# Kernel tuning notes

Hardware: AMD Instinct MI355X
Metric: run time of the kernel (lower is better)

The kernel has to match this reference:

```python
import jax, jax.numpy as jnp
import numpy as np

N_QUBITS = 18
LAYERS = 6
DATA_REUPLOADING = True


def _apply_1q(state, gate, q, n):
    # state: [2^n] complex, gate: [2,2] complex, acts on qubit q (big-endian)
    s = state.reshape(2 ** q, 2, 2 ** (n - q - 1))
    s = jnp.einsum('ab,ibj->iaj', gate, s)
    return s.reshape(-1)


def _apply_cz_adj(state, q, n):
    # CZ on adjacent qubits (q, q+1): flip sign of |..11..> amplitudes
    s = state.reshape(2 ** q, 2, 2, 2 ** (n - q - 2))
    s = s.at[:, 1, 1, :].multiply(-1.0)
    return s.reshape(-1)


def _rx(t):
    c = jnp.cos(t / 2).astype(jnp.complex64)
    s = (-1j * jnp.sin(t / 2)).astype(jnp.complex64)
    return jnp.stack([jnp.stack([c, s]), jnp.stack([s, c])])


def _ry(t):
    c = jnp.cos(t / 2).astype(jnp.complex64)
    s = jnp.sin(t / 2).astype(jnp.complex64)
    return jnp.stack([jnp.stack([c, -s]), jnp.stack([s, c])])


def _rz(t):
    em = jnp.exp(-1j * t.astype(jnp.complex64) / 2)
    ep = jnp.exp(1j * t.astype(jnp.complex64) / 2)
    z = jnp.zeros((), jnp.complex64)
    return jnp.stack([jnp.stack([em, z]), jnp.stack([z, ep])])


def _circuit(x, input_scaling, variational):
    # Hardware-efficient ansatz: RX(data) encoding, RY+RZ variational, CZ chain
    n = N_QUBITS
    state = jnp.zeros(2 ** n, jnp.complex64).at[0].set(1.0)
    for l in range(LAYERS):
        if l == 0 or DATA_REUPLOADING:
            for q in range(n):
                state = _apply_1q(state, _rx(input_scaling[l, q] * x[q]), q, n)
        for q in range(n):
            state = _apply_1q(state, _ry(variational[l, q]), q, n)
        for q in range(n):
            state = _apply_1q(state, _rz(variational[l, n + q]), q, n)
        for q in range(n - 1):
            state = _apply_cz_adj(state, q, n)
    return state


def setup_inputs() -> dict:
    key = jax.random.key(0)
    k1, k2, k3 = jax.random.split(key, 3)
    x1 = jax.random.normal(k1, (N_QUBITS,), jnp.float32)
    x2 = jax.random.normal(k2, (N_QUBITS,), jnp.float32)
    input_scaling = jnp.ones((LAYERS, N_QUBITS), jnp.float32)
    variational = (jax.random.uniform(k3, (LAYERS, 2 * N_QUBITS), jnp.float32)
                   * 2 * np.pi - np.pi)
    return {"x1": x1, "x2": x2, "input_scaling": input_scaling,
            "variational": variational}


def reference(x1, x2, input_scaling, variational):
    psi1 = _circuit(x1, input_scaling, variational)
    psi2 = _circuit(x2, input_scaling, variational)
    # projector |0><0| expectation of U(x2)^dagger U(x1)|0> == |<psi2|psi1>|^2
    ov = jnp.vdot(psi2, psi1)
    return (ov.real ** 2 + ov.imag ** 2).astype(jnp.float32)
```

## Files before the change

kernel.cpp:

```cpp
#include <hip/hip_runtime.h>
#include <math.h>


#define NQ      18
#define NSTATE  (1 << NQ)
#define TPB     512
#define MAGIC   0x5EED5EEDu

__device__ __forceinline__ int SW(int i) { return i ^ ((i >> 5) & 31); }

__device__ __forceinline__ float2 cmulf(float2 a, float2 b) {
    return make_float2(a.x * b.x - a.y * b.y, a.x * b.y + a.y * b.x);
}

__device__ __forceinline__ float lxor(float x, int j) {
    if (j == 0) {
        int v = __float_as_int(x);
        return __int_as_float(__builtin_amdgcn_update_dpp(v, v, 0xB1, 0xF, 0xF, false));
    }
    if (j == 1) {
        int v = __float_as_int(x);
        return __int_as_float(__builtin_amdgcn_update_dpp(v, v, 0x4E, 0xF, 0xF, false));
    }
    return __shfl_xor(x, 1 << j, 64);
}

__device__ __forceinline__ void cpair(
    float& a0r, float& a0i, float& a1r, float& a1i,
    float u00r, float u00i, float u01r, float u01i,
    float u10r, float u10i, float u11r, float u11i)
{
    float n0r = u00r * a0r - u00i * a0i + u01r * a1r - u01i * a1i;
    float n0i = u00r * a0i + u00i * a0r + u01r * a1i + u01i * a1r;
    float n1r = u10r * a0r - u10i * a0i + u11r * a1r - u11i * a1i;
    float n1i = u10r * a0i + u10i * a0r + u11r * a1i + u11i * a1r;
    a0r = n0r; a0i = n0i; a1r = n1r; a1i = n1i;
}

template<int RB>
__device__ __forceinline__ void reg_gate4(float (&ar)[4], float (&ai)[4],
                                          const float2* up)
{
    float u00r = up[0].x, u00i = up[0].y, u01r = up[1].x, u01i = up[1].y;
    float u10r = up[2].x, u10i = up[2].y, u11r = up[3].x, u11i = up[3].y;
#pragma unroll
    for (int r = 0; r < 4; ++r) {
        if (r & RB) continue;
        int r1 = r | RB;
        cpair(ar[r], ai[r], ar[r1], ai[r1],
              u00r, u00i, u01r, u01i, u10r, u10i, u11r, u11i);
    }
}

__device__ __forceinline__ void lane_gate4(float (&ar)[4], float (&ai)[4],
                                           const float2* up, int lane, int j)
{
    float u00r = up[0].x, u00i = up[0].y, u01r = up[1].x, u01i = up[1].y;
    float u10r = up[2].x, u10i = up[2].y, u11r = up[3].x, u11i = up[3].y;
    int side = (lane >> j) & 1;
    float car = side ? u11r : u00r, cai = side ? u11i : u00i;
    float cbr = side ? u10r : u01r, cbi = side ? u10i : u01i;
#pragma unroll
    for (int r = 0; r < 4; ++r) {
        float pr = lxor(ar[r], j);
        float pi = lxor(ai[r], j);
        float mr = ar[r], mi = ai[r];
        ar[r] = car * mr - cai * mi + cbr * pr - cbi * pi;
        ai[r] = car * mi + cai * mr + cbr * pi + cbi * pr;
    }
}

__global__ __launch_bounds__(TPB) void sim_kernel(
    float2* __restrict__ states,
    const float* __restrict__ x1, const float* __restrict__ x2,
    const float* __restrict__ iscale, const float* __restrict__ var,
    double* __restrict__ acc, unsigned* __restrict__ cnt,
    unsigned* __restrict__ flags, float* __restrict__ out)
{
    __shared__ float sre[2048], sim_[2048];
    __shared__ float2 sUa[5 * 11 * 4];
    __shared__ float2 sUb[5 * 11 * 4];
    __shared__ float2 sDa[6 * 4];
    __shared__ float2 sDb[11 * 4];
    __shared__ double wr[8], wi[8];

    int blk = blockIdx.x, t = threadIdx.x, lane = t & 63, wave = t >> 6;
    int c = blk >> 7, gc = blk & 127;
    int wv0 = wave & 1, wv1 = (wave >> 1) & 1, wv2 = (wave >> 2) & 1;
    const float* xv = c ? x2 : x1;

    if (blk == 0 && t == 0) {
        acc[0] = 0.0; acc[1] = 0.0; *cnt = 0u;
        __hip_atomic_store(&flags[128 * 16], MAGIC, __ATOMIC_RELEASE,
                           __HIP_MEMORY_SCOPE_AGENT);
    }

    if (t < 110) {
        int which = t >= 55;
        int tt = which ? t - 55 : t;
        int l = tt / 11, w = tt % 11;
        int q = which ? (17 - w) : (10 - w);
        float tx = iscale[l * NQ + q] * xv[q];
        float ty = var[l * 2 * NQ + q];
        float tz = var[l * 2 * NQ + NQ + q];
        float sx, cx, sy, cy, sz, cz;
        sincosf(tx * 0.5f, &sx, &cx);
        sincosf(ty * 0.5f, &sy, &cy);
        sincosf(tz * 0.5f, &sz, &cz);
        float m00r = cy * cx,  m00i =  sy * sx;
        float m01r = -sy * cx, m01i = -cy * sx;
        float m10r = sy * cx,  m10i = -cy * sx;
        float m11r = cy * cx,  m11i = -sy * sx;
        float2* up = which ? &sUb[(l * 11 + w) * 4] : &sUa[(l * 11 + w) * 4];
        up[0] = make_float2(m00r * cz + m00i * sz, m00i * cz - m00r * sz);
        up[1] = make_float2(m01r * cz + m01i * sz, m01i * cz - m01r * sz);
        up[2] = make_float2(m10r * cz - m10i * sz, m10i * cz + m10r * sz);
        up[3] = make_float2(m11r * cz - m11i * sz, m11i * cz + m11r * sz);
    } else if (t < 127) {
        int isb = t >= 116;
        int j = isb ? (t - 116) : (t - 110);
        int q = isb ? (17 - j) : (5 - j);
        float d = iscale[5 * NQ + q] * (x1[q] - x2[q]);
        float sn, cs;
        sincosf(d * 0.5f, &sn, &cs);
        float2* up = isb ? &sDb[j * 4] : &sDa[j * 4];
        up[0] = make_float2(cs, 0.f);  up[1] = make_float2(0.f, sn);
        up[2] = make_float2(0.f, sn);  up[3] = make_float2(cs, 0.f);
    }
    __syncthreads();

    float ar[4], ai[4];
    auto V1 = [&](int r) { return wv0 | ((r & 1) << 1) | (((r >> 1) & 1) << 2)
                                | (wv1 << 3) | (wv2 << 4) | (lane << 5); };
    auto V2 = [&](int r) { return wv0 | (wv1 << 1) | (wv2 << 2)
                                | ((r & 1) << 3) | (((r >> 1) & 1) << 4) | (lane << 5); };
    auto V3 = [&](int r) { return wv0 | (wv1 << 1) | ((r & 1) << 2)
                                | (((r >> 1) & 1) << 3) | (wv2 << 4) | (lane << 5); };
    auto T1 = [&](int r) { return lane | ((r & 1) << 6) | (((r >> 1) & 1) << 7)
                                | (wv0 << 8) | (wv1 << 9) | (wv2 << 10); };
    auto T2 = [&](int r) { return lane | (wv0 << 6) | (wv1 << 7)
                                | ((r & 1) << 8) | (((r >> 1) & 1) << 9) | (wv2 << 10); };
    auto T6 = [&](int r) { return lane | (wv0 << 6) | (wv1 << 7) | (wv2 << 8)
                                | ((r & 1) << 9) | (((r >> 1) & 1) << 10); };
    auto T8 = [&](int r) { return lane | (wv0 << 6) | (wv1 << 7)
                                | ((r & 1) << 8) | (wv2 << 9) | (((r >> 1) & 1) << 10); };
    auto rot = [&](auto from, auto to) {
#pragma unroll
        for (int r = 0; r < 4; ++r) { int s = SW(from(r)); sre[s] = ar[r]; sim_[s] = ai[r]; }
        __syncthreads();
#pragma unroll
        for (int r = 0; r < 4; ++r) { int s = SW(to(r)); ar[r] = sre[s]; ai[r] = sim_[s]; }
        __syncthreads();
    };
    auto Ua = [&](int l, int w) -> const float2* { return &sUa[(l * 11 + w) * 4]; };
    auto Ub = [&](int l, int w) -> const float2* { return &sUb[(l * 11 + w) * 4]; };
    auto czfold = [&](unsigned M, auto gidx) {
#pragma unroll
        for (int r = 0; r < 4; ++r) {
            int i = gidx(r);
            if (__popc(i & (i >> 1) & M) & 1) { ar[r] = -ar[r]; ai[r] = -ai[r]; }
        }
    };
    auto gV1 = [&](int r) { return V1(r) << 7; };
    auto gV2 = [&](int r) { return V2(r) << 7; };
    auto gV3 = [&](int r) { return V3(r) << 7; };
    auto gT1 = [&](int r) { return (gc << 11) | T1(r); };
    auto gT2 = [&](int r) { return (gc << 11) | T2(r); };
    auto gT6 = [&](int r) { return (gc << 11) | T6(r); };

    {
        float2 com = make_float2(1.f, 0.f);
        const float2* u0 = Ua(0, 0); com = cmulf(com, wv0 ? u0[2] : u0[0]);
        const float2* u3 = Ua(0, 3); com = cmulf(com, wv1 ? u3[2] : u3[0]);
        const float2* u4 = Ua(0, 4); com = cmulf(com, wv2 ? u4[2] : u4[0]);
#pragma unroll
        for (int j = 0; j < 6; ++j) {
            const float2* u = Ua(0, 5 + j);
            com = cmulf(com, ((lane >> j) & 1) ? u[2] : u[0]);
        }
        const float2* u1 = Ua(0, 1); const float2* u2 = Ua(0, 2);
#pragma unroll
        for (int r = 0; r < 4; ++r) {
            float2 f = cmulf((r & 1) ? u1[2] : u1[0], (r & 2) ? u2[2] : u2[0]);
            f = cmulf(com, f);
            ar[r] = f.x; ai[r] = f.y;
        }
    }
    czfold(0x1FF80u, gV1);
    reg_gate4<1>(ar, ai, Ua(1, 1));
    reg_gate4<2>(ar, ai, Ua(1, 2));
#pragma unroll
    for (int j = 0; j < 6; ++j) lane_gate4(ar, ai, Ua(1, 5 + j), lane, j);
    rot(V1, V2);
    reg_gate4<1>(ar, ai, Ua(1, 3));
    reg_gate4<2>(ar, ai, Ua(1, 4));
    czfold(0x1FF00u, gV2);
    reg_gate4<1>(ar, ai, Ua(2, 3));
    reg_gate4<2>(ar, ai, Ua(2, 4));
#pragma unroll
    for (int j = 0; j < 6; ++j) lane_gate4(ar, ai, Ua(2, 5 + j), lane, j);
    rot(V2, V3);
    reg_gate4<1>(ar, ai, Ua(2, 2));
    czfold(0x1FE00u, gV3);
    reg_gate4<2>(ar, ai, Ua(3, 3));
#pragma unroll
    for (int j = 0; j < 6; ++j) lane_gate4(ar, ai, Ua(3, 5 + j), lane, j);
    rot(V3, V2);
    reg_gate4<2>(ar, ai, Ua(3, 4));
    czfold(0x1FC00u, gV2);
    reg_gate4<2>(ar, ai, Ua(4, 4));
#pragma unroll
    for (int j = 0; j < 6; ++j) lane_gate4(ar, ai, Ua(4, 5 + j), lane, j);
    rot(V2, V1);
    czfold(0x1F800u, gV1);
    if (c == 1) {
#pragma unroll
        for (int j = 0; j < 6; ++j) lane_gate4(ar, ai, &sDa[j * 4], lane, j);
    }
#pragma unroll
    for (int r = 0; r < 4; ++r) { int s = SW(V1(r)); sre[s] = ar[r]; sim_[s] = ai[r]; }
    __syncthreads();
#pragma unroll
    for (int r = 0; r < 4; ++r) {
        int x = T1(r);
        if ((x & 127) == 0) {
            int Wv = (gc << 4) | (x >> 7);
            int s = SW(Wv);
            ar[r] = sre[s]; ai[r] = sim_[s];
        } else { ar[r] = 0.f; ai[r] = 0.f; }
    }
    __syncthreads();

#pragma unroll
    for (int j = 0; j < 6; ++j) lane_gate4(ar, ai, Ub(0, j), lane, j);
    reg_gate4<1>(ar, ai, Ub(0, 6));
    czfold(0x7Fu, gT1);
#pragma unroll
    for (int j = 0; j < 6; ++j) lane_gate4(ar, ai, Ub(1, j), lane, j);
    reg_gate4<1>(ar, ai, Ub(1, 6));
    reg_gate4<2>(ar, ai, Ub(1, 7));
    rot(T1, T2);
    czfold(0xFFu, gT2);
#pragma unroll
    for (int j = 0; j < 6; ++j) lane_gate4(ar, ai, Ub(2, j), lane, j);
    reg_gate4<1>(ar, ai, Ub(2, 8));
    rot(T2, T1);
    reg_gate4<1>(ar, ai, Ub(2, 6));
    reg_gate4<2>(ar, ai, Ub(2, 7));
    czfold(0x1FFu, gT1);
#pragma unroll
    for (int j = 0; j < 6; ++j) lane_gate4(ar, ai, Ub(3, j), lane, j);
    reg_gate4<1>(ar, ai, Ub(3, 6));
    reg_gate4<2>(ar, ai, Ub(3, 7));
    rot(T1, T2);
    reg_gate4<1>(ar, ai, Ub(3, 8));
    reg_gate4<2>(ar, ai, Ub(3, 9));
    czfold(0x3FFu, gT2);
#pragma unroll
    for (int j = 0; j < 6; ++j) lane_gate4(ar, ai, Ub(4, j), lane, j);
    reg_gate4<1>(ar, ai, Ub(4, 8));
    reg_gate4<2>(ar, ai, Ub(4, 9));
    rot(T2, T1);
    reg_gate4<1>(ar, ai, Ub(4, 6));
    reg_gate4<2>(ar, ai, Ub(4, 7));
    czfold(0xE0u, gT1);
    rot(T1, T6);
    reg_gate4<2>(ar, ai, Ub(4, 10));
    czfold(0x71Fu, gT6);

    if (c == 0) {
#pragma unroll
        for (int r = 0; r < 4; ++r) {
            int i = (gc << 11) | T6(r);
            states[i] = make_float2(ar[r], ai[r]);
        }
        __syncthreads();
        if (t == 0) {
            __hip_atomic_store(&flags[gc * 16], MAGIC, __ATOMIC_RELEASE,
                               __HIP_MEMORY_SCOPE_AGENT);
        }
    } else {
#pragma unroll
        for (int j = 0; j < 5; ++j) lane_gate4(ar, ai, &sDb[j * 4], lane, j);
        reg_gate4<1>(ar, ai, &sDb[9 * 4]);
        reg_gate4<2>(ar, ai, &sDb[10 * 4]);
        rot(T6, T1);
        lane_gate4(ar, ai, &sDb[5 * 4], lane, 5);
        reg_gate4<1>(ar, ai, &sDb[6 * 4]);
        reg_gate4<2>(ar, ai, &sDb[7 * 4]);
        rot(T1, T8);
        reg_gate4<1>(ar, ai, &sDb[8 * 4]);

        float d6 = iscale[5 * NQ + 6] * (x1[6] - x2[6]);
        float sn6, cs6;
        sincosf(d6 * 0.5f, &sn6, &cs6);
        float cf = cs6, sf = sn6;

        if (t == 0) {
            while (__hip_atomic_load(&flags[gc * 16], __ATOMIC_RELAXED,
                                     __HIP_MEMORY_SCOPE_AGENT) != MAGIC)
                __builtin_amdgcn_s_sleep(1);
            while (__hip_atomic_load(&flags[(gc ^ 1) * 16], __ATOMIC_RELAXED,
                                     __HIP_MEMORY_SCOPE_AGENT) != MAGIC)
                __builtin_amdgcn_s_sleep(1);
            while (__hip_atomic_load(&flags[128 * 16], __ATOMIC_RELAXED,
                                     __HIP_MEMORY_SCOPE_AGENT) != MAGIC)
                __builtin_amdgcn_s_sleep(1);
            __builtin_amdgcn_fence(__ATOMIC_ACQUIRE, "agent");
        }
        __syncthreads();

        double accr = 0.0, acci = 0.0;
#pragma unroll
        for (int r = 0; r < 4; ++r) {
            int i = (gc << 11) | T8(r);
            float2 p1 = states[i];
            float2 pp = states[i ^ 2048];
            float gr = cf * p1.x + sf * pp.y;
            float gi = cf * p1.y - sf * pp.x;
            accr += (double)ar[r] * gr + (double)ai[r] * gi;
            acci += (double)ar[r] * gi - (double)ai[r] * gr;
        }
        for (int o = 32; o > 0; o >>= 1) {
            accr += __shfl_down(accr, o, 64);
            acci += __shfl_down(acci, o, 64);
        }
        if (lane == 0) { wr[wave] = accr; wi[wave] = acci; }
        __syncthreads();
        if (t == 0) {
            double br = 0.0, bi = 0.0;
#pragma unroll
            for (int w = 0; w < 8; ++w) { br += wr[w]; bi += wi[w]; }
            atomicAdd(&acc[0], br);
            atomicAdd(&acc[1], bi);
            __threadfence();
            unsigned old = atomicAdd(cnt, 1u);
            if (old == 127u) {
                double fr = atomicAdd(&acc[0], 0.0);
                double fi = atomicAdd(&acc[1], 0.0);
                out[0] = (float)(fr * fr + fi * fi);
            }
        }
    }
}

extern "C" void kernel_launch(void* const* d_in, const int* in_sizes, int n_in,
                              void* d_out, int out_size, void* d_ws, size_t ws_size,
                              hipStream_t stream)
{
    const float* x1 = (const float*)d_in[0];
    const float* x2 = (const float*)d_in[1];
    const float* iscale = (const float*)d_in[2];
    const float* var = (const float*)d_in[3];
    float* out = (float*)d_out;

    double*   acc    = (double*)((char*)d_ws + 8192);
    unsigned* cnt    = (unsigned*)((char*)d_ws + 8320);
    unsigned* flags  = (unsigned*)((char*)d_ws + 16384);
    float2*   states = (float2*)((char*)d_ws + 65536);

    sim_kernel<<<256, TPB, 0, stream>>>(states, x1, x2, iscale, var,
                                        acc, cnt, flags, out);
}
```

Baseline: 84.94 us.

## Double block size to 1024 threads with two amplitudes per thread

Each block now runs 1024 threads, and each thread holds 2 amplitudes instead of 4, so the per-thread serial gate chain is shorter and each CU has more waves for latency hiding. Qubits that used to live in registers are now reached through extra LDS rotations, so the schedule gains more rot steps and more barriers. The trailing __syncthreads inside rot is also dropped to save a barrier per rotation. That risks a write-after-read race on the shared buffers when one rotation is followed closely by the next.

```diff
diff --git a/kernel.cpp b/kernel.cpp
--- a/kernel.cpp
+++ b/kernel.cpp
@@ -4,7 +4,7 @@
 
 #define NQ      18
 #define NSTATE  (1 << NQ)
-#define TPB     512
+#define TPB     1024
 #define MAGIC   0x5EED5EEDu
 
 __device__ __forceinline__ int SW(int i) { return i ^ ((i >> 5) & 31); }
@@ -37,22 +37,14 @@
     a0r = n0r; a0i = n0i; a1r = n1r; a1i = n1i;
 }
 
-template<int RB>
-__device__ __forceinline__ void reg_gate4(float (&ar)[4], float (&ai)[4],
+__device__ __forceinline__ void reg_gate2(float (&ar)[2], float (&ai)[2],
                                           const float2* up)
 {
-    float u00r = up[0].x, u00i = up[0].y, u01r = up[1].x, u01i = up[1].y;
-    float u10r = up[2].x, u10i = up[2].y, u11r = up[3].x, u11i = up[3].y;
-#pragma unroll
-    for (int r = 0; r < 4; ++r) {
-        if (r & RB) continue;
-        int r1 = r | RB;
-        cpair(ar[r], ai[r], ar[r1], ai[r1],
-              u00r, u00i, u01r, u01i, u10r, u10i, u11r, u11i);
-    }
-}
-
-__device__ __forceinline__ void lane_gate4(float (&ar)[4], float (&ai)[4],
+    cpair(ar[0], ai[0], ar[1], ai[1],
+          up[0].x, up[0].y, up[1].x, up[1].y, up[2].x, up[2].y, up[3].x, up[3].y);
+}
+
+__device__ __forceinline__ void lane_gate2(float (&ar)[2], float (&ai)[2],
                                            const float2* up, int lane, int j)
 {
     float u00r = up[0].x, u00i = up[0].y, u01r = up[1].x, u01i = up[1].y;
@@ -61,7 +53,7 @@
     float car = side ? u11r : u00r, cai = side ? u11i : u00i;
     float cbr = side ? u10r : u01r, cbi = side ? u10i : u01i;
 #pragma unroll
-    for (int r = 0; r < 4; ++r) {
+    for (int r = 0; r < 2; ++r) {
         float pr = lxor(ar[r], j);
         float pi = lxor(ai[r], j);
         float mr = ar[r], mi = ai[r];
@@ -82,11 +74,12 @@
     __shared__ float2 sUb[5 * 11 * 4];
     __shared__ float2 sDa[6 * 4];
     __shared__ float2 sDb[11 * 4];
-    __shared__ double wr[8], wi[8];
+    __shared__ double wr[16], wi[16];
 
     int blk = blockIdx.x, t = threadIdx.x, lane = t & 63, wave = t >> 6;
     int c = blk >> 7, gc = blk & 127;
-    int wv0 = wave & 1, wv1 = (wave >> 1) & 1, wv2 = (wave >> 2) & 1;
+    int wv0 = wave & 1, wv1 = (wave >> 1) & 1, wv2 = (wave >> 2) & 1,
+        wv3 = (wave >> 3) & 1;
     const float* xv = c ? x2 : x1;
 
     if (blk == 0 && t == 0) {
@@ -129,34 +122,37 @@
     }
     __syncthreads();
 
-    float ar[4], ai[4];
-    auto V1 = [&](int r) { return wv0 | ((r & 1) << 1) | (((r >> 1) & 1) << 2)
-                                | (wv1 << 3) | (wv2 << 4) | (lane << 5); };
-    auto V2 = [&](int r) { return wv0 | (wv1 << 1) | (wv2 << 2)
-                                | ((r & 1) << 3) | (((r >> 1) & 1) << 4) | (lane << 5); };
-    auto V3 = [&](int r) { return wv0 | (wv1 << 1) | ((r & 1) << 2)
-                                | (((r >> 1) & 1) << 3) | (wv2 << 4) | (lane << 5); };
-    auto T1 = [&](int r) { return lane | ((r & 1) << 6) | (((r >> 1) & 1) << 7)
-                                | (wv0 << 8) | (wv1 << 9) | (wv2 << 10); };
-    auto T2 = [&](int r) { return lane | (wv0 << 6) | (wv1 << 7)
-                                | ((r & 1) << 8) | (((r >> 1) & 1) << 9) | (wv2 << 10); };
-    auto T6 = [&](int r) { return lane | (wv0 << 6) | (wv1 << 7) | (wv2 << 8)
-                                | ((r & 1) << 9) | (((r >> 1) & 1) << 10); };
-    auto T8 = [&](int r) { return lane | (wv0 << 6) | (wv1 << 7)
-                                | ((r & 1) << 8) | (wv2 << 9) | (((r >> 1) & 1) << 10); };
+    float ar[2], ai[2];
+    auto V1 = [&](int r) { return wv0 | (r << 1) | (wv1 << 2) | (wv2 << 3)
+                                | (wv3 << 4) | (lane << 5); };
+    auto V2 = [&](int r) { return wv0 | (wv1 << 1) | (r << 2) | (wv2 << 3)
+                                | (wv3 << 4) | (lane << 5); };
+    auto V3 = [&](int r) { return wv0 | (wv1 << 1) | (wv2 << 2) | (r << 3)
+                                | (wv3 << 4) | (lane << 5); };
+    auto V4 = [&](int r) { return wv0 | (wv1 << 1) | (wv2 << 2) | (wv3 << 3)
+                                | (r << 4) | (lane << 5); };
+    auto T6  = [&](int r) { return lane | (r << 6) | (wv0 << 7) | (wv1 << 8)
+                                 | (wv2 << 9) | (wv3 << 10); };
+    auto T7  = [&](int r) { return lane | (wv0 << 6) | (r << 7) | (wv1 << 8)
+                                 | (wv2 << 9) | (wv3 << 10); };
+    auto T8  = [&](int r) { return lane | (wv0 << 6) | (wv1 << 7) | (r << 8)
+                                 | (wv2 << 9) | (wv3 << 10); };
+    auto T9  = [&](int r) { return lane | (wv0 << 6) | (wv1 << 7) | (wv2 << 8)
+                                 | (r << 9) | (wv3 << 10); };
+    auto T10 = [&](int r) { return lane | (wv0 << 6) | (wv1 << 7) | (wv2 << 8)
+                                 | (wv3 << 9) | (r << 10); };
     auto rot = [&](auto from, auto to) {
 #pragma unroll
-        for (int r = 0; r < 4; ++r) { int s = SW(from(r)); sre[s] = ar[r]; sim_[s] = ai[r]; }
+        for (int r = 0; r < 2; ++r) { int s = SW(from(r)); sre[s] = ar[r]; sim_[s] = ai[r]; }
         __syncthreads();
 #pragma unroll
-        for (int r = 0; r < 4; ++r) { int s = SW(to(r)); ar[r] = sre[s]; ai[r] = sim_[s]; }
-        __syncthreads();
+        for (int r = 0; r < 2; ++r) { int s = SW(to(r)); ar[r] = sre[s]; ai[r] = sim_[s]; }
     };
     auto Ua = [&](int l, int w) -> const float2* { return &sUa[(l * 11 + w) * 4]; };
     auto Ub = [&](int l, int w) -> const float2* { return &sUb[(l * 11 + w) * 4]; };
     auto czfold = [&](unsigned M, auto gidx) {
 #pragma unroll
-        for (int r = 0; r < 4; ++r) {
+        for (int r = 0; r < 2; ++r) {
             int i = gidx(r);
             if (__popc(i & (i >> 1) & M) & 1) { ar[r] = -ar[r]; ai[r] = -ai[r]; }
         }
@@ -164,65 +160,69 @@
     auto gV1 = [&](int r) { return V1(r) << 7; };
     auto gV2 = [&](int r) { return V2(r) << 7; };
     auto gV3 = [&](int r) { return V3(r) << 7; };
-    auto gT1 = [&](int r) { return (gc << 11) | T1(r); };
-    auto gT2 = [&](int r) { return (gc << 11) | T2(r); };
+    auto gV4 = [&](int r) { return V4(r) << 7; };
     auto gT6 = [&](int r) { return (gc << 11) | T6(r); };
+    auto gT7 = [&](int r) { return (gc << 11) | T7(r); };
+    auto gT8 = [&](int r) { return (gc << 11) | T8(r); };
+    auto gT9 = [&](int r) { return (gc << 11) | T9(r); };
 
     {
         float2 com = make_float2(1.f, 0.f);
         const float2* u0 = Ua(0, 0); com = cmulf(com, wv0 ? u0[2] : u0[0]);
-        const float2* u3 = Ua(0, 3); com = cmulf(com, wv1 ? u3[2] : u3[0]);
-        const float2* u4 = Ua(0, 4); com = cmulf(com, wv2 ? u4[2] : u4[0]);
+        const float2* u2 = Ua(0, 2); com = cmulf(com, wv1 ? u2[2] : u2[0]);
+        const float2* u3 = Ua(0, 3); com = cmulf(com, wv2 ? u3[2] : u3[0]);
+        const float2* u4 = Ua(0, 4); com = cmulf(com, wv3 ? u4[2] : u4[0]);
 #pragma unroll
         for (int j = 0; j < 6; ++j) {
             const float2* u = Ua(0, 5 + j);
             com = cmulf(com, ((lane >> j) & 1) ? u[2] : u[0]);
         }
-        const float2* u1 = Ua(0, 1); const float2* u2 = Ua(0, 2);
-#pragma unroll
-        for (int r = 0; r < 4; ++r) {
-            float2 f = cmulf((r & 1) ? u1[2] : u1[0], (r & 2) ? u2[2] : u2[0]);
-            f = cmulf(com, f);
+        const float2* u1 = Ua(0, 1);
+#pragma unroll
+        for (int r = 0; r < 2; ++r) {
+            float2 f = cmulf(com, r ? u1[2] : u1[0]);
             ar[r] = f.x; ai[r] = f.y;
         }
     }
     czfold(0x1FF80u, gV1);
-    reg_gate4<1>(ar, ai, Ua(1, 1));
-    reg_gate4<2>(ar, ai, Ua(1, 2));
-#pragma unroll
-    for (int j = 0; j < 6; ++j) lane_gate4(ar, ai, Ua(1, 5 + j), lane, j);
+    reg_gate2(ar, ai, Ua(1, 1));
+#pragma unroll
+    for (int j = 0; j < 6; ++j) lane_gate2(ar, ai, Ua(1, 5 + j), lane, j);
     rot(V1, V2);
-    reg_gate4<1>(ar, ai, Ua(1, 3));
-    reg_gate4<2>(ar, ai, Ua(1, 4));
-    czfold(0x1FF00u, gV2);
-    reg_gate4<1>(ar, ai, Ua(2, 3));
-    reg_gate4<2>(ar, ai, Ua(2, 4));
-#pragma unroll
-    for (int j = 0; j < 6; ++j) lane_gate4(ar, ai, Ua(2, 5 + j), lane, j);
+    reg_gate2(ar, ai, Ua(1, 2));
     rot(V2, V3);
-    reg_gate4<1>(ar, ai, Ua(2, 2));
+    reg_gate2(ar, ai, Ua(1, 3));
+    rot(V3, V4);
+    reg_gate2(ar, ai, Ua(1, 4));
+    czfold(0x1FF00u, gV4);
+    reg_gate2(ar, ai, Ua(2, 4));
+#pragma unroll
+    for (int j = 0; j < 6; ++j) lane_gate2(ar, ai, Ua(2, 5 + j), lane, j);
+    rot(V4, V2);
+    reg_gate2(ar, ai, Ua(2, 2));
+    rot(V2, V3);
+    reg_gate2(ar, ai, Ua(2, 3));
     czfold(0x1FE00u, gV3);
-    reg_gate4<2>(ar, ai, Ua(3, 3));
-#pragma unroll
-    for (int j = 0; j < 6; ++j) lane_gate4(ar, ai, Ua(3, 5 + j), lane, j);
-    rot(V3, V2);
-    reg_gate4<2>(ar, ai, Ua(3, 4));
-    czfold(0x1FC00u, gV2);
-    reg_gate4<2>(ar, ai, Ua(4, 4));
-#pragma unroll
-    for (int j = 0; j < 6; ++j) lane_gate4(ar, ai, Ua(4, 5 + j), lane, j);
-    rot(V2, V1);
-    czfold(0x1F800u, gV1);
+    reg_gate2(ar, ai, Ua(3, 3));
+#pragma unroll
+    for (int j = 0; j < 6; ++j) lane_gate2(ar, ai, Ua(3, 5 + j), lane, j);
+    rot(V3, V4);
+    reg_gate2(ar, ai, Ua(3, 4));
+    czfold(0x1FC00u, gV4);
+    reg_gate2(ar, ai, Ua(4, 4));
+#pragma unroll
+    for (int j = 0; j < 6; ++j) lane_gate2(ar, ai, Ua(4, 5 + j), lane, j);
+    czfold(0x1F800u, gV4);
     if (c == 1) {
 #pragma unroll
-        for (int j = 0; j < 6; ++j) lane_gate4(ar, ai, &sDa[j * 4], lane, j);
-    }
-#pragma unroll
-    for (int r = 0; r < 4; ++r) { int s = SW(V1(r)); sre[s] = ar[r]; sim_[s] = ai[r]; }
+        for (int j = 0; j < 6; ++j) lane_gate2(ar, ai, &sDa[j * 4], lane, j);
+    }
+#pragma unroll
+    for (int r = 0; r < 2; ++r) { int s = SW(V4(r)); sre[s] = ar[r]; sim_[s] = ai[r]; }
     __syncthreads();
 #pragma unroll
-    for (int r = 0; r < 4; ++r) {
-        int x = T1(r);
+    for (int r = 0; r < 2; ++r) {
+        int x = T6(r);
         if ((x & 127) == 0) {
             int Wv = (gc << 4) | (x >> 7);
             int s = SW(Wv);
@@ -232,45 +232,49 @@
     __syncthreads();
 
 #pragma unroll
-    for (int j = 0; j < 6; ++j) lane_gate4(ar, ai, Ub(0, j), lane, j);
-    reg_gate4<1>(ar, ai, Ub(0, 6));
-    czfold(0x7Fu, gT1);
-#pragma unroll
-    for (int j = 0; j < 6; ++j) lane_gate4(ar, ai, Ub(1, j), lane, j);
-    reg_gate4<1>(ar, ai, Ub(1, 6));
-    reg_gate4<2>(ar, ai, Ub(1, 7));
-    rot(T1, T2);
-    czfold(0xFFu, gT2);
-#pragma unroll
-    for (int j = 0; j < 6; ++j) lane_gate4(ar, ai, Ub(2, j), lane, j);
-    reg_gate4<1>(ar, ai, Ub(2, 8));
-    rot(T2, T1);
-    reg_gate4<1>(ar, ai, Ub(2, 6));
-    reg_gate4<2>(ar, ai, Ub(2, 7));
-    czfold(0x1FFu, gT1);
-#pragma unroll
-    for (int j = 0; j < 6; ++j) lane_gate4(ar, ai, Ub(3, j), lane, j);
-    reg_gate4<1>(ar, ai, Ub(3, 6));
-    reg_gate4<2>(ar, ai, Ub(3, 7));
-    rot(T1, T2);
-    reg_gate4<1>(ar, ai, Ub(3, 8));
-    reg_gate4<2>(ar, ai, Ub(3, 9));
-    czfold(0x3FFu, gT2);
-#pragma unroll
-    for (int j = 0; j < 6; ++j) lane_gate4(ar, ai, Ub(4, j), lane, j);
-    reg_gate4<1>(ar, ai, Ub(4, 8));
-    reg_gate4<2>(ar, ai, Ub(4, 9));
-    rot(T2, T1);
-    reg_gate4<1>(ar, ai, Ub(4, 6));
-    reg_gate4<2>(ar, ai, Ub(4, 7));
-    czfold(0xE0u, gT1);
-    rot(T1, T6);
-    reg_gate4<2>(ar, ai, Ub(4, 10));
-    czfold(0x71Fu, gT6);
+    for (int j = 0; j < 6; ++j) lane_gate2(ar, ai, Ub(0, j), lane, j);
+    reg_gate2(ar, ai, Ub(0, 6));
+    czfold(0x7Fu, gT6);
+#pragma unroll
+    for (int j = 0; j < 6; ++j) lane_gate2(ar, ai, Ub(1, j), lane, j);
+    reg_gate2(ar, ai, Ub(1, 6));
+    rot(T6, T7);
+    reg_gate2(ar, ai, Ub(1, 7));
+    czfold(0xFFu, gT7);
+    reg_gate2(ar, ai, Ub(2, 7));
+#pragma unroll
+    for (int j = 0; j < 6; ++j) lane_gate2(ar, ai, Ub(2, j), lane, j);
+    rot(T7, T8);
+    reg_gate2(ar, ai, Ub(2, 8));
+    rot(T8, T6);
+    reg_gate2(ar, ai, Ub(2, 6));
+    czfold(0x1FFu, gT6);
+    reg_gate2(ar, ai, Ub(3, 6));
+#pragma unroll
+    for (int j = 0; j < 6; ++j) lane_gate2(ar, ai, Ub(3, j), lane, j);
+    rot(T6, T7);
+    reg_gate2(ar, ai, Ub(3, 7));
+    rot(T7, T8);
+    reg_gate2(ar, ai, Ub(3, 8));
+    rot(T8, T9);
+    reg_gate2(ar, ai, Ub(3, 9));
+    czfold(0x3FFu, gT9);
+    reg_gate2(ar, ai, Ub(4, 9));
+#pragma unroll
+    for (int j = 0; j < 6; ++j) lane_gate2(ar, ai, Ub(4, j), lane, j);
+    rot(T9, T10);
+    reg_gate2(ar, ai, Ub(4, 10));
+    rot(T10, T8);
+    reg_gate2(ar, ai, Ub(4, 8));
+    rot(T8, T7);
+    reg_gate2(ar, ai, Ub(4, 7));
+    rot(T7, T6);
+    reg_gate2(ar, ai, Ub(4, 6));
+    czfold(0x7FFu, gT6);
 
     if (c == 0) {
 #pragma unroll
-        for (int r = 0; r < 4; ++r) {
+        for (int r = 0; r < 2; ++r) {
             int i = (gc << 11) | T6(r);
             states[i] = make_float2(ar[r], ai[r]);
         }
@@ -281,15 +285,16 @@
         }
     } else {
 #pragma unroll
-        for (int j = 0; j < 5; ++j) lane_gate4(ar, ai, &sDb[j * 4], lane, j);
-        reg_gate4<1>(ar, ai, &sDb[9 * 4]);
-        reg_gate4<2>(ar, ai, &sDb[10 * 4]);
-        rot(T6, T1);
-        lane_gate4(ar, ai, &sDb[5 * 4], lane, 5);
-        reg_gate4<1>(ar, ai, &sDb[6 * 4]);
-        reg_gate4<2>(ar, ai, &sDb[7 * 4]);
-        rot(T1, T8);
-        reg_gate4<1>(ar, ai, &sDb[8 * 4]);
+        for (int j = 0; j < 6; ++j) lane_gate2(ar, ai, &sDb[j * 4], lane, j);
+        reg_gate2(ar, ai, &sDb[6 * 4]);
+        rot(T6, T7);
+        reg_gate2(ar, ai, &sDb[7 * 4]);
+        rot(T7, T8);
+        reg_gate2(ar, ai, &sDb[8 * 4]);
+        rot(T8, T9);
+        reg_gate2(ar, ai, &sDb[9 * 4]);
+        rot(T9, T10);
+        reg_gate2(ar, ai, &sDb[10 * 4]);
 
         float d6 = iscale[5 * NQ + 6] * (x1[6] - x2[6]);
         float sn6, cs6;
@@ -312,8 +317,8 @@
 
         double accr = 0.0, acci = 0.0;
 #pragma unroll
-        for (int r = 0; r < 4; ++r) {
-            int i = (gc << 11) | T8(r);
+        for (int r = 0; r < 2; ++r) {
+            int i = (gc << 11) | T10(r);
             float2 p1 = states[i];
             float2 pp = states[i ^ 2048];
             float gr = cf * p1.x + sf * pp.y;
@@ -330,7 +335,7 @@
         if (t == 0) {
             double br = 0.0, bi = 0.0;
 #pragma unroll
-            for (int w = 0; w < 8; ++w) { br += wr[w]; bi += wi[w]; }
+            for (int w = 0; w < 16; ++w) { br += wr[w]; bi += wi[w]; }
             atomicAdd(&acc[0], br);
             atomicAdd(&acc[1], bi);
             __threadfence();
```

Measured after the change: 85.68 us. About the same (+0.9%).
